# Optimization experiments

Hardware: AMD Instinct MI355X
Metric: run time of the kernel (lower is better)

The kernel has to match this reference:

```python
import jax, jax.numpy as jnp
import numpy as np

B, FDIM = 8192, 2048
S = 10000          # number of sign nodes
D = 100            # num diseases
E = 500000         # number of 'finding' edges
ETA = 0.01


def setup_inputs() -> dict:
    key = jax.random.key(0)
    k1, k2, k3, k4, k5 = jax.random.split(key, 5)
    grad_output_batch = jax.random.normal(k1, (B, FDIM), dtype=jnp.float32)
    # similarity of each sign node per sample (0 => sign not found)
    sims = jax.random.uniform(k2, (B, S), dtype=jnp.float32)
    edge_weight = jax.random.uniform(k3, (E,), dtype=jnp.float32)
    edge_src = jax.random.randint(k4, (E,), 0, D)   # disease node per edge
    edge_dst = jax.random.randint(k5, (E,), 0, S)   # sign node per edge
    return {
        "grad_output_batch": grad_output_batch,
        "sims": sims,
        "edge_weight": edge_weight,
        "edge_src": edge_src,
        "edge_dst": edge_dst,
        "num_diseases": D,
    }


def reference(grad_output_batch, sims, edge_weight, edge_src, edge_dst, num_diseases):
    # Scatter-add edge weights into disease x sign matrix A[d, s]
    A = jnp.zeros((num_diseases, sims.shape[1]), dtype=sims.dtype)
    A = A.at[edge_src, edge_dst].add(edge_weight)
    # Per-sample gradient norm g_i = ||grad_output_batch[i]||_2
    g = jnp.linalg.norm(grad_output_batch, axis=1)            # [B]
    # nudges[i, d] = eta * g_i * sum_s sims[i, s] * A[d, s]
    nudges = ETA * g[:, None] * jnp.einsum('bs,ds->bd', sims, A)
    return nudges
```

## Files before the change

kernel.cpp:

```cpp
#include <hip/hip_runtime.h>
#include <hip/hip_bf16.h>

#define B_DIM   8192
#define FDIM    2048
#define S_DIM   10000
#define D_DIM   100
#define E_NUM   500000
#define ETA     0.01f

#define DPAD    112
#define NT      7
#define KSTEPS  313
#define KSPLIT  8
#define MROWS   128
#define KBLK    1252

typedef float  f32x4  __attribute__((ext_vector_type(4)));
typedef short  s16x8  __attribute__((ext_vector_type(8)));
typedef __bf16 bf16x8 __attribute__((ext_vector_type(8)));

__device__ inline unsigned short f2bf_bits(float x) {
    unsigned int u = __float_as_uint(x);
    unsigned int r = u + 0x7FFFu + ((u >> 16) & 1u);
    return (unsigned short)(r >> 16);
}

__global__ void scatter_kernel(const float* __restrict__ ew,
                               const int* __restrict__ esrc,
                               const int* __restrict__ edst,
                               float* __restrict__ A) {
    int e = blockIdx.x * 256 + threadIdx.x;
    if (e < E_NUM) {
        atomicAdd(&A[(size_t)esrc[e] * S_DIM + edst[e]], ew[e]);
    }
}

__global__ void build_asw_kernel(const float* __restrict__ A,
                                 unsigned short* __restrict__ Asw) {
    int t = blockIdx.x * 256 + threadIdx.x;
    int kb  = t / 896;
    int rem = t - kb * 896;
    int d   = rem >> 3;
    int s   = kb * 8 + (rem & 7);
    float v = (d < D_DIM && s < S_DIM) ? A[d * S_DIM + s] : 0.f;
    Asw[t] = f2bf_bits(v);
}

__global__ void norm_kernel(const float* __restrict__ go, float* __restrict__ g) {
    int wave = threadIdx.x >> 6;
    int lane = threadIdx.x & 63;
    int row  = blockIdx.x * 4 + wave;
    const f32x4* p = (const f32x4*)(go + (size_t)row * FDIM);
    float s = 0.f;
#pragma unroll
    for (int j = 0; j < 8; ++j) {
        f32x4 v = __builtin_nontemporal_load(p + lane + 64 * j);
        s += v[0]*v[0] + v[1]*v[1] + v[2]*v[2] + v[3]*v[3];
    }
#pragma unroll
    for (int off = 32; off; off >>= 1) s += __shfl_xor(s, off);
    if (lane == 0) g[row] = sqrtf(s);
}

__device__ inline s16x8 cvt_a(f32x4 f0, f32x4 f1) {
    bf16x8 abf;
    abf[0] = (__bf16)f0[0]; abf[1] = (__bf16)f0[1];
    abf[2] = (__bf16)f0[2]; abf[3] = (__bf16)f0[3];
    abf[4] = (__bf16)f1[0]; abf[5] = (__bf16)f1[1];
    abf[6] = (__bf16)f1[2]; abf[7] = (__bf16)f1[3];
    return __builtin_bit_cast(s16x8, abf);
}

__global__ __launch_bounds__(512, 4)
void gemm_kernel(const float* __restrict__ sims,
                 const unsigned short* __restrict__ Asw,
                 float* __restrict__ part) {
    __shared__ unsigned short buf[2][3584];
    const int tid  = threadIdx.x;
    const int wave = tid >> 6;
    const int lane = tid & 63;
    const int lhi  = lane >> 4;
    const int llo  = lane & 15;

    const int kb = blockIdx.x & 7;
    const int rb = blockIdx.x >> 3;
    const int t0 = (KSTEPS * kb) >> 3;
    const int t1 = (KSTEPS * (kb + 1)) >> 3;
    const int nsteps = t1 - t0;

    const int row0 = rb * MROWS + wave * 16;
    const float* srow = sims + (size_t)(row0 + llo) * S_DIM + 8 * lhi;

    f32x4 acc[NT];
#pragma unroll
    for (int n = 0; n < NT; ++n) acc[n] = 0.f;

    if (tid < 448) {
        s16x8 v = *(const s16x8*)(Asw + (size_t)t0 * 3584 + tid * 8);
        *(s16x8*)&buf[0][tid * 8] = v;
    }
    f32x4 f0, f1;
    {
        const f32x4* p = (const f32x4*)(srow + t0 * 32);
        f0 = p[0]; f1 = p[1];
    }
    __syncthreads();

    for (int i = 0; i < nsteps; ++i) {
        const int t = t0 + i;
        const int cur = i & 1;

        if (i + 1 < nsteps && tid < 448) {
            s16x8 v = *(const s16x8*)(Asw + (size_t)(t + 1) * 3584 + tid * 8);
            *(s16x8*)&buf[cur ^ 1][tid * 8] = v;
        }

        f32x4 n0 = 0.f, n1 = 0.f;
        {
            const int kn = (t + 1) * 32 + 8 * lhi;
            if (i + 1 < nsteps && kn <= S_DIM - 8) {
                const f32x4* p = (const f32x4*)(srow + (size_t)(t + 1) * 32);
                n0 = p[0]; n1 = p[1];
            }
        }

        const unsigned short* bb = &buf[cur][lhi * 896 + llo * 8];
        s16x8 b0 = *(const s16x8*)(bb);
        s16x8 b1 = *(const s16x8*)(bb + 128);
        s16x8 b2 = *(const s16x8*)(bb + 256);
        s16x8 b3 = *(const s16x8*)(bb + 384);
        s16x8 b4 = *(const s16x8*)(bb + 512);
        s16x8 b5 = *(const s16x8*)(bb + 640);
        s16x8 b6 = *(const s16x8*)(bb + 768);

        s16x8 a = cvt_a(f0, f1);
        acc[0] = __builtin_amdgcn_mfma_f32_16x16x32_bf16(a, b0, acc[0], 0, 0, 0);
        acc[1] = __builtin_amdgcn_mfma_f32_16x16x32_bf16(a, b1, acc[1], 0, 0, 0);
        acc[2] = __builtin_amdgcn_mfma_f32_16x16x32_bf16(a, b2, acc[2], 0, 0, 0);
        acc[3] = __builtin_amdgcn_mfma_f32_16x16x32_bf16(a, b3, acc[3], 0, 0, 0);
        acc[4] = __builtin_amdgcn_mfma_f32_16x16x32_bf16(a, b4, acc[4], 0, 0, 0);
        acc[5] = __builtin_amdgcn_mfma_f32_16x16x32_bf16(a, b5, acc[5], 0, 0, 0);
        acc[6] = __builtin_amdgcn_mfma_f32_16x16x32_bf16(a, b6, acc[6], 0, 0, 0);

        f0 = n0; f1 = n1;
        __syncthreads();
    }

    float* pslab = part + (size_t)kb * (B_DIM * D_DIM);
    const int rbase = row0 + lhi * 4;
#pragma unroll
    for (int n = 0; n < NT; ++n) {
        const int col = n * 16 + llo;
        if (col < D_DIM) {
#pragma unroll
            for (int r = 0; r < 4; ++r)
                pslab[(size_t)(rbase + r) * D_DIM + col] = acc[n][r];
        }
    }
}

__global__ void reduce_kernel(const float* __restrict__ part,
                              const float* __restrict__ g,
                              float* __restrict__ out) {
    int idx = blockIdx.x * 256 + threadIdx.x;
    if (idx < B_DIM * D_DIM) {
        float s = 0.f;
#pragma unroll
        for (int kb = 0; kb < KSPLIT; ++kb)
            s += part[(size_t)kb * (B_DIM * D_DIM) + idx];
        int i = idx / D_DIM;
        out[idx] = ETA * g[i] * s;
    }
}

extern "C" void kernel_launch(void* const* d_in, const int* in_sizes, int n_in,
                              void* d_out, int out_size, void* d_ws, size_t ws_size,
                              hipStream_t stream) {
    const float* grad = (const float*)d_in[0];
    const float* sims = (const float*)d_in[1];
    const float* ew   = (const float*)d_in[2];
    const int*   esrc = (const int*)d_in[3];
    const int*   edst = (const int*)d_in[4];
    float* out = (float*)d_out;

    char* ws = (char*)d_ws;
    float*          A    = (float*)(ws);
    unsigned short* Asw  = (unsigned short*)(ws + (4 << 20));
    float*          g    = (float*)(ws + (7 << 20));
    float*          part = (float*)(ws + (8 << 20));

    hipMemsetAsync(A, 0, (size_t)D_DIM * S_DIM * sizeof(float), stream);

    scatter_kernel  <<<(E_NUM + 255) / 256, 256, 0, stream>>>(ew, esrc, edst, A);
    build_asw_kernel<<<(KBLK * DPAD * 8) / 256, 256, 0, stream>>>(A, Asw);
    norm_kernel     <<<B_DIM / 4, 256, 0, stream>>>(grad, g);
    gemm_kernel     <<<64 * KSPLIT, 512, 0, stream>>>(sims, Asw, part);
    reduce_kernel   <<<(B_DIM * D_DIM + 255) / 256, 256, 0, stream>>>(part, g, out);
}
```

Before: 517.2 us.

## Deepen GEMM prefetch pipeline and halve block rows for more blocks

The GEMM kernel now uses 256-thread blocks covering 64 rows, launched as twice as many blocks, so more workgroups can be resident and the grid is spread more evenly. The sims stream is prefetched two k-steps ahead using nontemporal loads. The B-tile global loads are issued before the MFMAs, with the LDS stores deferred until after them, so load latency overlaps compute. This costs more registers, and each block now stages a larger share of the shared B tile relative to its work.

```diff
diff --git a/kernel.cpp b/kernel.cpp
--- a/kernel.cpp
+++ b/kernel.cpp
@@ -12,7 +12,7 @@
 #define NT      7
 #define KSTEPS  313
 #define KSPLIT  8
-#define MROWS   128
+#define MROWS   64
 #define KBLK    1252
 
 typedef float  f32x4  __attribute__((ext_vector_type(4)));
@@ -71,7 +71,7 @@
     return __builtin_bit_cast(s16x8, abf);
 }
 
-__global__ __launch_bounds__(512, 4)
+__global__ __launch_bounds__(256, 4)
 void gemm_kernel(const float* __restrict__ sims,
                  const unsigned short* __restrict__ Asw,
                  float* __restrict__ part) {
@@ -95,14 +95,20 @@
 #pragma unroll
     for (int n = 0; n < NT; ++n) acc[n] = 0.f;
 
-    if (tid < 448) {
-        s16x8 v = *(const s16x8*)(Asw + (size_t)t0 * 3584 + tid * 8);
-        *(s16x8*)&buf[0][tid * 8] = v;
-    }
-    f32x4 f0, f1;
+    if (tid < 224) {
+        const s16x8* src = (const s16x8*)(Asw + (size_t)t0 * 3584 + tid * 16);
+        s16x8 v0 = src[0], v1 = src[1];
+        *(s16x8*)&buf[0][tid * 16]     = v0;
+        *(s16x8*)&buf[0][tid * 16 + 8] = v1;
+    }
+    f32x4 c0, c1, n0, n1;
     {
         const f32x4* p = (const f32x4*)(srow + t0 * 32);
-        f0 = p[0]; f1 = p[1];
+        c0 = __builtin_nontemporal_load(p);
+        c1 = __builtin_nontemporal_load(p + 1);
+        const f32x4* q = (const f32x4*)(srow + (t0 + 1) * 32);
+        n0 = __builtin_nontemporal_load(q);
+        n1 = __builtin_nontemporal_load(q + 1);
     }
     __syncthreads();
 
@@ -110,18 +116,18 @@
         const int t = t0 + i;
         const int cur = i & 1;
 
-        if (i + 1 < nsteps && tid < 448) {
-            s16x8 v = *(const s16x8*)(Asw + (size_t)(t + 1) * 3584 + tid * 8);
-            *(s16x8*)&buf[cur ^ 1][tid * 8] = v;
-        }
-
-        f32x4 n0 = 0.f, n1 = 0.f;
-        {
-            const int kn = (t + 1) * 32 + 8 * lhi;
-            if (i + 1 < nsteps && kn <= S_DIM - 8) {
-                const f32x4* p = (const f32x4*)(srow + (size_t)(t + 1) * 32);
-                n0 = p[0]; n1 = p[1];
-            }
+        s16x8 sv0, sv1;
+        const bool do_stage = (i + 1 < nsteps) && (tid < 224);
+        if (do_stage) {
+            const s16x8* src = (const s16x8*)(Asw + (size_t)(t + 1) * 3584 + tid * 16);
+            sv0 = src[0]; sv1 = src[1];
+        }
+
+        f32x4 m0 = 0.f, m1 = 0.f;
+        if (i + 2 < nsteps && (t + 2) * 32 + 8 * lhi <= S_DIM - 8) {
+            const f32x4* p = (const f32x4*)(srow + (size_t)(t + 2) * 32);
+            m0 = __builtin_nontemporal_load(p);
+            m1 = __builtin_nontemporal_load(p + 1);
         }
 
         const unsigned short* bb = &buf[cur][lhi * 896 + llo * 8];
@@ -133,7 +139,7 @@
         s16x8 b5 = *(const s16x8*)(bb + 640);
         s16x8 b6 = *(const s16x8*)(bb + 768);
 
-        s16x8 a = cvt_a(f0, f1);
+        s16x8 a = cvt_a(c0, c1);
         acc[0] = __builtin_amdgcn_mfma_f32_16x16x32_bf16(a, b0, acc[0], 0, 0, 0);
         acc[1] = __builtin_amdgcn_mfma_f32_16x16x32_bf16(a, b1, acc[1], 0, 0, 0);
         acc[2] = __builtin_amdgcn_mfma_f32_16x16x32_bf16(a, b2, acc[2], 0, 0, 0);
@@ -142,7 +148,12 @@
         acc[5] = __builtin_amdgcn_mfma_f32_16x16x32_bf16(a, b5, acc[5], 0, 0, 0);
         acc[6] = __builtin_amdgcn_mfma_f32_16x16x32_bf16(a, b6, acc[6], 0, 0, 0);
 
-        f0 = n0; f1 = n1;
+        if (do_stage) {
+            *(s16x8*)&buf[cur ^ 1][tid * 16]     = sv0;
+            *(s16x8*)&buf[cur ^ 1][tid * 16 + 8] = sv1;
+        }
+
+        c0 = n0; c1 = n1; n0 = m0; n1 = m1;
         __syncthreads();
     }
 
@@ -194,6 +205,6 @@
     scatter_kernel  <<<(E_NUM + 255) / 256, 256, 0, stream>>>(ew, esrc, edst, A);
     build_asw_kernel<<<(KBLK * DPAD * 8) / 256, 256, 0, stream>>>(A, Asw);
     norm_kernel     <<<B_DIM / 4, 256, 0, stream>>>(grad, g);
-    gemm_kernel     <<<64 * KSPLIT, 512, 0, stream>>>(sims, Asw, part);
+    gemm_kernel     <<<128 * KSPLIT, 256, 0, stream>>>(sims, Asw, part);
     reduce_kernel   <<<(B_DIM * D_DIM + 255) / 256, 256, 0, stream>>>(part, g, out);
 }
```

New measurement: 547.5 us. 5.9% more time.

## Drop LDS staging of B operand; read Asw directly from global per wave

Applied to the files above, without the earlier changes.

The GEMM kernel no longer stages the bf16 disease matrix through double-buffered shared memory with a block barrier each step. Each wave now loads its B fragments straight from global memory, where the small matrix is expected to sit in L2. Blocks shrink to 4 waves covering 64 rows, and the grid doubles so total coverage stays the same. Sims loads become nontemporal. The aim is to remove per-step barriers and LDS traffic, at the cost of more global/L2 reads of B and a B load latency that is no longer hidden.

```diff
diff --git a/kernel.cpp b/kernel.cpp
--- a/kernel.cpp
+++ b/kernel.cpp
@@ -12,7 +12,7 @@
 #define NT      7
 #define KSTEPS  313
 #define KSPLIT  8
-#define MROWS   128
+#define MROWS   64
 #define KBLK    1252
 
 typedef float  f32x4  __attribute__((ext_vector_type(4)));
@@ -71,11 +71,10 @@
     return __builtin_bit_cast(s16x8, abf);
 }
 
-__global__ __launch_bounds__(512, 4)
+__global__ __launch_bounds__(256, 4)
 void gemm_kernel(const float* __restrict__ sims,
                  const unsigned short* __restrict__ Asw,
                  float* __restrict__ part) {
-    __shared__ unsigned short buf[2][3584];
     const int tid  = threadIdx.x;
     const int wave = tid >> 6;
     const int lane = tid & 63;
@@ -95,36 +94,24 @@
 #pragma unroll
     for (int n = 0; n < NT; ++n) acc[n] = 0.f;
 
-    if (tid < 448) {
-        s16x8 v = *(const s16x8*)(Asw + (size_t)t0 * 3584 + tid * 8);
-        *(s16x8*)&buf[0][tid * 8] = v;
+    f32x4 c0, c1;
+    {
+        const f32x4* p = (const f32x4*)(srow + (size_t)t0 * 32);
+        c0 = __builtin_nontemporal_load(p);
+        c1 = __builtin_nontemporal_load(p + 1);
     }
-    f32x4 f0, f1;
-    {
-        const f32x4* p = (const f32x4*)(srow + t0 * 32);
-        f0 = p[0]; f1 = p[1];
-    }
-    __syncthreads();
 
     for (int i = 0; i < nsteps; ++i) {
         const int t = t0 + i;
-        const int cur = i & 1;
 
-        if (i + 1 < nsteps && tid < 448) {
-            s16x8 v = *(const s16x8*)(Asw + (size_t)(t + 1) * 3584 + tid * 8);
-            *(s16x8*)&buf[cur ^ 1][tid * 8] = v;
+        f32x4 n0 = 0.f, n1 = 0.f;
+        if (i + 1 < nsteps && (t + 1) * 32 + 8 * lhi <= S_DIM - 8) {
+            const f32x4* p = (const f32x4*)(srow + (size_t)(t + 1) * 32);
+            n0 = __builtin_nontemporal_load(p);
+            n1 = __builtin_nontemporal_load(p + 1);
         }
 
-        f32x4 n0 = 0.f, n1 = 0.f;
-        {
-            const int kn = (t + 1) * 32 + 8 * lhi;
-            if (i + 1 < nsteps && kn <= S_DIM - 8) {
-                const f32x4* p = (const f32x4*)(srow + (size_t)(t + 1) * 32);
-                n0 = p[0]; n1 = p[1];
-            }
-        }
-
-        const unsigned short* bb = &buf[cur][lhi * 896 + llo * 8];
+        const unsigned short* bb = Asw + ((size_t)(4 * t + lhi) * DPAD + llo) * 8;
         s16x8 b0 = *(const s16x8*)(bb);
         s16x8 b1 = *(const s16x8*)(bb + 128);
         s16x8 b2 = *(const s16x8*)(bb + 256);
@@ -133,7 +120,7 @@
         s16x8 b5 = *(const s16x8*)(bb + 640);
         s16x8 b6 = *(const s16x8*)(bb + 768);
 
-        s16x8 a = cvt_a(f0, f1);
+        s16x8 a = cvt_a(c0, c1);
         acc[0] = __builtin_amdgcn_mfma_f32_16x16x32_bf16(a, b0, acc[0], 0, 0, 0);
         acc[1] = __builtin_amdgcn_mfma_f32_16x16x32_bf16(a, b1, acc[1], 0, 0, 0);
         acc[2] = __builtin_amdgcn_mfma_f32_16x16x32_bf16(a, b2, acc[2], 0, 0, 0);
@@ -142,8 +129,7 @@
         acc[5] = __builtin_amdgcn_mfma_f32_16x16x32_bf16(a, b5, acc[5], 0, 0, 0);
         acc[6] = __builtin_amdgcn_mfma_f32_16x16x32_bf16(a, b6, acc[6], 0, 0, 0);
 
-        f0 = n0; f1 = n1;
-        __syncthreads();
+        c0 = n0; c1 = n1;
     }
 
     float* pslab = part + (size_t)kb * (B_DIM * D_DIM);
@@ -194,6 +180,6 @@
     scatter_kernel  <<<(E_NUM + 255) / 256, 256, 0, stream>>>(ew, esrc, edst, A);
     build_asw_kernel<<<(KBLK * DPAD * 8) / 256, 256, 0, stream>>>(A, Asw);
     norm_kernel     <<<B_DIM / 4, 256, 0, stream>>>(grad, g);
-    gemm_kernel     <<<64 * KSPLIT, 512, 0, stream>>>(sims, Asw, part);
+    gemm_kernel     <<<128 * KSPLIT, 256, 0, stream>>>(sims, Asw, part);
     reduce_kernel   <<<(B_DIM * D_DIM + 255) / 256, 256, 0, stream>>>(part, g, out);
 }
```

Result: slower. 564.2 us (+9.1%).
